# Kernel optimization log

Hardware: AMD Instinct MI355X
Metric: run time of the kernel (lower is better)

Reference implementation:

```python
import jax, jax.numpy as jnp
import numpy as np

N = 50000   # full-order mesh size
n = 10      # latent dim
MU = 32     # neighbourhood / window size
B = 8       # batch of snapshots


def setup_inputs() -> dict:
    key = jax.random.key(0)
    ks = jax.random.split(key, 6)
    x = jax.random.normal(ks[0], (B, N), jnp.float32)
    enc_w = jax.random.normal(ks[1], (n, N), jnp.float32) * 0.01  # torch Linear weight [n, N]
    enc_b = jax.random.normal(ks[2], (n,), jnp.float32) * 0.01
    decoder = jax.random.uniform(ks[3], (n, N), jnp.float32, minval=-0.01, maxval=0.01)
    bandwidth_layers = jax.random.uniform(ks[4], (n, n, N), jnp.float32, minval=-0.01, maxval=0.01)
    neighbours = jax.random.randint(ks[5], (N, MU), 0, N, jnp.int32)
    return dict(x=x, enc_w=enc_w, enc_b=enc_b, decoder=decoder,
                bandwidth_layers=bandwidth_layers, neighbours=neighbours)


def reference(x, enc_w, enc_b, decoder, bandwidth_layers, neighbours):
    mu = neighbours.shape[1]
    # encode: torch Linear -> x @ W.T + b                      [B, n]
    encoded = x @ enc_w.T + enc_b
    # bandwidths: bmm(encoded.repeat(n,1,1), bw).permute(1,0,2) -> sigmoid   [B, n, N]
    w = jax.nn.sigmoid(jnp.einsum('bk,ikp->bip', encoded, bandwidth_layers))
    # bubble window per scalar w: relu(1 - x^2/(w*mu)^2), normalized over mu  [B, n, N, mu]
    xs2 = (jnp.arange(mu, dtype=x.dtype) ** 2)  # [mu]
    win = jax.nn.relu(1.0 - xs2 / (w[..., None] * mu) ** 2)
    win = win / jnp.sum(win, axis=-1, keepdims=True)
    # gather decoder rows at each node's neighbours            [n, N, mu]
    gathered = jnp.take(decoder, neighbours, axis=1)
    # smooth_vec: sum over neighbourhood                       [B, n, N]
    smoothed = jnp.einsum('ipm,bipm->bip', gathered, win)
    # final bmm: encoded [B,1,n] @ smoothed [B,n,N] -> [B,N]
    return jnp.einsum('bi,bip->bp', encoded, smoothed)
```

## Files before the change

### kernel.cpp

```cpp
#include <hip/hip_runtime.h>
#include <hip/hip_bf16.h>

#define N_NODES 50000
#define NLAT 10
#define MU 32
#define BATCH 8
#define CHUNK 2000
#define NCHUNK 25
#define ENC_BLOCKS (BATCH * NLAT * NCHUNK)
#define TR_BLOCKS ((N_NODES + 255) / 256)
#define DT_STRIDE 16
#define NPB 64
#define NBR_PAD 36

typedef float v2f __attribute__((ext_vector_type(2)));

static __device__ __forceinline__ v2f v2_fma(v2f a, v2f b, v2f c) {
#if __has_builtin(__builtin_elementwise_fma)
    return __builtin_elementwise_fma(a, b, c);
#else
    v2f r; r[0] = fmaf(a[0], b[0], c[0]); r[1] = fmaf(a[1], b[1], c[1]); return r;
#endif
}
static __device__ __forceinline__ v2f v2_max0(v2f a) {
#if __has_builtin(__builtin_elementwise_max)
    v2f z = {0.0f, 0.0f};
    return __builtin_elementwise_max(a, z);
#else
    v2f r; r[0] = fmaxf(a[0], 0.0f); r[1] = fmaxf(a[1], 0.0f); return r;
#endif
}

__global__ __launch_bounds__(256) void encode_a_transpose(
    const float* __restrict__ x, const float* __restrict__ enc_w,
    const float* __restrict__ dec,
    float* __restrict__ partial, float* __restrict__ dec_t) {
    const int bid = blockIdx.x;
    if (bid < ENC_BLOCKS) {
        const int c  = bid % NCHUNK;
        const int bi = bid / NCHUNK;
        const int b = bi / NLAT, i = bi % NLAT;
        const float4* xr = (const float4*)(x + (size_t)b * N_NODES + c * CHUNK);
        const float4* wr = (const float4*)(enc_w + (size_t)i * N_NODES + c * CHUNK);
        float part = 0.0f;
        for (int q = threadIdx.x; q < CHUNK / 4; q += 256) {
            float4 xv = xr[q], wv = wr[q];
            part += xv.x * wv.x + xv.y * wv.y + xv.z * wv.z + xv.w * wv.w;
        }
        for (int off = 32; off; off >>= 1) part += __shfl_down(part, off, 64);
        __shared__ float s[4];
        if ((threadIdx.x & 63) == 0) s[threadIdx.x >> 6] = part;
        __syncthreads();
        if (threadIdx.x == 0) partial[bid] = (s[0] + s[1]) + (s[2] + s[3]);
    } else {
        const int p = (bid - ENC_BLOCKS) * 256 + threadIdx.x;
        if (p >= N_NODES) return;
        float v[DT_STRIDE];
        #pragma unroll
        for (int i = 0; i < NLAT; ++i) v[i] = dec[(size_t)i * N_NODES + p];
        #pragma unroll
        for (int i = NLAT; i < DT_STRIDE; ++i) v[i] = 0.0f;
        float4* dst = (float4*)(dec_t + (size_t)p * DT_STRIDE);
        #pragma unroll
        for (int q = 0; q < 4; ++q)
            dst[q] = make_float4(v[4*q], v[4*q+1], v[4*q+2], v[4*q+3]);
    }
}

__global__ __launch_bounds__(512, 6) void nrbs_main_kernel(
    const float* __restrict__ dec_t,
    const float* __restrict__ bw,
    const int*   __restrict__ nbr,
    const float* __restrict__ partial,
    const float* __restrict__ enc_b,
    float*       __restrict__ out) {
    __shared__ float s_enc[BATCH * NLAT];
    __shared__ float s_inv[NLAT][NPB][BATCH];
    __shared__ int   s_tm[NPB];
    __shared__ int   s_nbr[NPB][NBR_PAD];
    const int tid   = threadIdx.x;
    const int node0 = blockIdx.x * NPB;

    if (tid < BATCH * NLAT) {
        float s = 0.0f;
        #pragma unroll
        for (int c = 0; c < NCHUNK; ++c) s += partial[tid * NCHUNK + c];
        s_enc[tid] = s + enc_b[tid % NLAT];
    }
    if (tid < NPB) s_tm[tid] = 0;
    {
        const int nodeS = tid >> 3, ch = tid & 7;
        int4 v = make_int4(0, 0, 0, 0);
        if (node0 + nodeS < N_NODES)
            v = ((const int4*)(nbr + (size_t)(node0 + nodeS) * MU))[ch];
        *(int4*)&s_nbr[nodeS][ch * 4] = v;
    }
    __syncthreads();

    {
        const int g    = tid >> 6;
        const int lane = tid & 63;
        const int p    = node0 + lane;
        if (p < N_NODES) {
            float tloc = 0.0f;
            {
                const int i = g;
                float bwv[NLAT];
                #pragma unroll
                for (int k = 0; k < NLAT; ++k)
                    bwv[k] = bw[((size_t)(i * NLAT + k)) * N_NODES + p];
                float invv[BATCH];
                #pragma unroll
                for (int b = 0; b < BATCH; ++b) {
                    float z = 0.0f;
                    #pragma unroll
                    for (int k = 0; k < NLAT; ++k)
                        z = fmaf(s_enc[b * NLAT + k], bwv[k], z);
                    const float sg = 1.0f / (1.0f + __expf(-z));
                    const float t  = sg * (float)MU;
                    tloc = fmaxf(tloc, t);
                    invv[b] = __builtin_amdgcn_rcpf(t * t);
                }
                float4* dst = (float4*)&s_inv[i][lane][0];
                dst[0] = make_float4(invv[0], invv[1], invv[2], invv[3]);
                dst[1] = make_float4(invv[4], invv[5], invv[6], invv[7]);
            }
            {
                const int i  = 8 + (g >> 2);
                const int b0 = (g & 3) * 2;
                float bwv[NLAT];
                #pragma unroll
                for (int k = 0; k < NLAT; ++k)
                    bwv[k] = bw[((size_t)(i * NLAT + k)) * N_NODES + p];
                float iv2[2];
                #pragma unroll
                for (int h = 0; h < 2; ++h) {
                    float z = 0.0f;
                    #pragma unroll
                    for (int k = 0; k < NLAT; ++k)
                        z = fmaf(s_enc[(b0 + h) * NLAT + k], bwv[k], z);
                    const float sg = 1.0f / (1.0f + __expf(-z));
                    const float t  = sg * (float)MU;
                    tloc = fmaxf(tloc, t);
                    iv2[h] = __builtin_amdgcn_rcpf(t * t);
                }
                *(float2*)&s_inv[i][lane][b0] = make_float2(iv2[0], iv2[1]);
            }
            atomicMax(&s_tm[lane], __float_as_int(tloc));
        }
    }
    __syncthreads();

    const int node  = tid >> 3;
    const int ipair = tid & 7;
    const int p     = node0 + node;
    const int i0    = 2 * ipair;
    const bool act  = (ipair < 5) && (p < N_NODES);

    v2f inv2[2][4], asum[2][4], ssum[2][4];
    #pragma unroll
    for (int ii = 0; ii < 2; ++ii)
        #pragma unroll
        for (int b2 = 0; b2 < 4; ++b2) {
            inv2[ii][b2] = (v2f){0.0f, 0.0f};
            asum[ii][b2] = (v2f){0.0f, 0.0f};
            ssum[ii][b2] = (v2f){0.0f, 0.0f};
        }
    int mcap = 0;
    if (act) {
        #pragma unroll
        for (int ii = 0; ii < 2; ++ii) {
            const float4* iv = (const float4*)&s_inv[i0 + ii][node][0];
            const float4 a = iv[0], c = iv[1];
            inv2[ii][0] = (v2f){a.x, a.y}; inv2[ii][1] = (v2f){a.z, a.w};
            inv2[ii][2] = (v2f){c.x, c.y}; inv2[ii][3] = (v2f){c.z, c.w};
        }
        mcap = min(MU, (int)__int_as_float(s_tm[node]) + 1);
    }
    const int mcap4 = (mcap + 3) & ~3;

    const v2f one = {1.0f, 1.0f};
    const float* __restrict__ bp = dec_t + i0;

    auto step = [&](int m, v2f g2) {
        const float m2f = (float)(m * m);
        const v2f nm2 = {-m2f, -m2f};
        #pragma unroll
        for (int ii = 0; ii < 2; ++ii) {
            const v2f gg = {g2[ii], g2[ii]};
            #pragma unroll
            for (int b2 = 0; b2 < 4; ++b2) {
                const v2f win = v2_max0(v2_fma(nm2, inv2[ii][b2], one));
                ssum[ii][b2] += win;
                asum[ii][b2] = v2_fma(gg, win, asum[ii][b2]);
            }
        }
    };

    for (int mb = 0; mb < mcap4; mb += 4) {
        const int4 na = *(const int4*)&s_nbr[node][mb];
        const v2f g0 = *(const v2f*)(bp + (size_t)na.x * DT_STRIDE);
        const v2f g1 = *(const v2f*)(bp + (size_t)na.y * DT_STRIDE);
        const v2f g2 = *(const v2f*)(bp + (size_t)na.z * DT_STRIDE);
        const v2f g3 = *(const v2f*)(bp + (size_t)na.w * DT_STRIDE);
        step(mb + 0, g0); step(mb + 1, g1);
        step(mb + 2, g2); step(mb + 3, g3);
    }

    float r[BATCH];
    #pragma unroll
    for (int b2 = 0; b2 < 4; ++b2)
        #pragma unroll
        for (int h = 0; h < 2; ++h) {
            const int b = 2 * b2 + h;
            r[b] = act ? s_enc[b * NLAT + i0]     * asum[0][b2][h] *
                             __builtin_amdgcn_rcpf(ssum[0][b2][h]) +
                         s_enc[b * NLAT + i0 + 1] * asum[1][b2][h] *
                             __builtin_amdgcn_rcpf(ssum[1][b2][h])
                       : 0.0f;
        }
    #pragma unroll
    for (int mask = 1; mask < 8; mask <<= 1)
        #pragma unroll
        for (int b = 0; b < BATCH; ++b)
            r[b] += __shfl_xor(r[b], mask, 8);

    if (p < N_NODES)
        out[(size_t)ipair * N_NODES + p] = r[ipair];
}

extern "C" void kernel_launch(void* const* d_in, const int* in_sizes, int n_in,
                              void* d_out, int out_size, void* d_ws, size_t ws_size,
                              hipStream_t stream) {
    const float* x       = (const float*)d_in[0];
    const float* enc_w   = (const float*)d_in[1];
    const float* enc_b   = (const float*)d_in[2];
    const float* decoder = (const float*)d_in[3];
    const float* bwl     = (const float*)d_in[4];
    const int*   nbr     = (const int*)d_in[5];
    float* out = (float*)d_out;

    float* partial = (float*)((char*)d_ws + 1024);
    float* dec_t   = (float*)((char*)d_ws + 65536);

    encode_a_transpose<<<ENC_BLOCKS + TR_BLOCKS, 256, 0, stream>>>(
        x, enc_w, decoder, partial, dec_t);

    const int blocks = (N_NODES + NPB - 1) / NPB;
    nrbs_main_kernel<<<blocks, 512, 0, stream>>>(
        dec_t, bwl, nbr, partial, enc_b, out);
}
```

Baseline: 106.4 us.

## Restructure encoder GEMV to reuse weight and input loads across batch and latents

The encoder partial-dot-product stage now has each block handle a 1000-column chunk for all 10 latent rows and 4 batch rows at once, instead of one (batch, latent, chunk) triple per block. This removes the redundant re-reading of x and enc_w across 2000 blocks, keeping the weight row slices in registers across batches. In exchange it launches far fewer encode blocks, does many more cross-lane shuffle reductions, and doubles the number of partials the main kernel must sum.

```diff
diff --git a/kernel.cpp b/kernel.cpp
--- a/kernel.cpp
+++ b/kernel.cpp
@@ -5,9 +5,9 @@
 #define NLAT 10
 #define MU 32
 #define BATCH 8
-#define CHUNK 2000
-#define NCHUNK 25
-#define ENC_BLOCKS (BATCH * NLAT * NCHUNK)
+#define CH2 1000
+#define NCH2 50
+#define ENC2_BLOCKS (NCH2 * 2)
 #define TR_BLOCKS ((N_NODES + 255) / 256)
 #define DT_STRIDE 16
 #define NPB 64
@@ -36,24 +36,57 @@
     const float* __restrict__ dec,
     float* __restrict__ partial, float* __restrict__ dec_t) {
     const int bid = blockIdx.x;
-    if (bid < ENC_BLOCKS) {
-        const int c  = bid % NCHUNK;
-        const int bi = bid / NCHUNK;
-        const int b = bi / NLAT, i = bi % NLAT;
-        const float4* xr = (const float4*)(x + (size_t)b * N_NODES + c * CHUNK);
-        const float4* wr = (const float4*)(enc_w + (size_t)i * N_NODES + c * CHUNK);
-        float part = 0.0f;
-        for (int q = threadIdx.x; q < CHUNK / 4; q += 256) {
-            float4 xv = xr[q], wv = wr[q];
-            part += xv.x * wv.x + xv.y * wv.y + xv.z * wv.z + xv.w * wv.w;
-        }
-        for (int off = 32; off; off >>= 1) part += __shfl_down(part, off, 64);
-        __shared__ float s[4];
-        if ((threadIdx.x & 63) == 0) s[threadIdx.x >> 6] = part;
+    if (bid < ENC2_BLOCKS) {
+        const int c  = bid >> 1;
+        const int b0 = (bid & 1) * 4;
+        const int q  = threadIdx.x;
+        float acc[4][NLAT];
+        #pragma unroll
+        for (int j = 0; j < 4; ++j)
+            #pragma unroll
+            for (int i = 0; i < NLAT; ++i) acc[j][i] = 0.0f;
+        if (q < CH2 / 4) {
+            float4 wv[NLAT];
+            #pragma unroll
+            for (int i = 0; i < NLAT; ++i)
+                wv[i] = ((const float4*)(enc_w + (size_t)i * N_NODES + c * CH2))[q];
+            #pragma unroll
+            for (int j = 0; j < 4; ++j) {
+                const float4 xv =
+                    ((const float4*)(x + (size_t)(b0 + j) * N_NODES + c * CH2))[q];
+                #pragma unroll
+                for (int i = 0; i < NLAT; ++i)
+                    acc[j][i] = fmaf(xv.x, wv[i].x,
+                                fmaf(xv.y, wv[i].y,
+                                fmaf(xv.z, wv[i].z,
+                                fmaf(xv.w, wv[i].w, acc[j][i]))));
+            }
+        }
+        #pragma unroll
+        for (int j = 0; j < 4; ++j)
+            #pragma unroll
+            for (int i = 0; i < NLAT; ++i)
+                #pragma unroll
+                for (int off = 32; off; off >>= 1)
+                    acc[j][i] += __shfl_down(acc[j][i], off, 64);
+        __shared__ float s_red[4][40];
+        if ((threadIdx.x & 63) == 0) {
+            const int w = threadIdx.x >> 6;
+            #pragma unroll
+            for (int j = 0; j < 4; ++j)
+                #pragma unroll
+                for (int i = 0; i < NLAT; ++i)
+                    s_red[w][j * NLAT + i] = acc[j][i];
+        }
         __syncthreads();
-        if (threadIdx.x == 0) partial[bid] = (s[0] + s[1]) + (s[2] + s[3]);
+        if (threadIdx.x < 40) {
+            const float s = (s_red[0][threadIdx.x] + s_red[1][threadIdx.x]) +
+                            (s_red[2][threadIdx.x] + s_red[3][threadIdx.x]);
+            const int j = threadIdx.x / NLAT, i = threadIdx.x % NLAT;
+            partial[(size_t)((b0 + j) * NLAT + i) * NCH2 + c] = s;
+        }
     } else {
-        const int p = (bid - ENC_BLOCKS) * 256 + threadIdx.x;
+        const int p = (bid - ENC2_BLOCKS) * 256 + threadIdx.x;
         if (p >= N_NODES) return;
         float v[DT_STRIDE];
         #pragma unroll
@@ -84,7 +117,7 @@
     if (tid < BATCH * NLAT) {
         float s = 0.0f;
         #pragma unroll
-        for (int c = 0; c < NCHUNK; ++c) s += partial[tid * NCHUNK + c];
+        for (int c = 0; c < NCH2; ++c) s += partial[tid * NCH2 + c];
         s_enc[tid] = s + enc_b[tid % NLAT];
     }
     if (tid < NPB) s_tm[tid] = 0;
@@ -243,7 +276,7 @@
     float* partial = (float*)((char*)d_ws + 1024);
     float* dec_t   = (float*)((char*)d_ws + 65536);
 
-    encode_a_transpose<<<ENC_BLOCKS + TR_BLOCKS, 256, 0, stream>>>(
+    encode_a_transpose<<<ENC2_BLOCKS + TR_BLOCKS, 256, 0, stream>>>(
         x, enc_w, decoder, partial, dec_t);
 
     const int blocks = (N_NODES + NPB - 1) / NPB;
```

Result: no change. 107.9 us (+1.5%).
